# Optimization experiments

Hardware: AMD Instinct MI355X
Metric: run time of the kernel (lower is better)

## Reference

```python
import jax, jax.numpy as jnp
import numpy as np

B, L, NT = 4, 512, 20
H, DK, DM = 6, 10, 60  # heads, d_k, d_model (=embedding_dim+1)
ED = 59


def setup_inputs() -> dict:
    key = jax.random.key(0)
    ks = jax.random.split(key, 12)
    # event_seqs[..., 0] = event times (increasing), event_seqs[..., 1] = event type id stored as float
    times = jnp.cumsum(jax.random.uniform(ks[0], (B, L + 1)), axis=1)
    types = jax.random.randint(ks[1], (B, L + 1), 0, NT).astype(jnp.float32)
    event_seqs = jnp.stack([times, types], axis=-1)  # [B, L+1, 2]
    # causal (subsequent) mask, no padding -> lower-triangular [B, L, L]
    src_mask = jnp.broadcast_to(jnp.tril(jnp.ones((L, L), dtype=bool)), (B, L, L))
    w = lambda k, s: jax.random.normal(k, s, dtype=jnp.float32) * 0.1
    return dict(
        event_seqs=event_seqs, src_mask=src_mask,
        embed_w=w(ks[2], (ED, NT)),
        q_w=w(ks[3], (DM, DM)), q_b=jnp.zeros((DM,), jnp.float32),
        k_w=w(ks[4], (DM, DM)), k_b=jnp.zeros((DM,), jnp.float32),
        v_w=w(ks[5], (DM, DM)), v_b=jnp.zeros((DM,), jnp.float32),
        alpha_w=w(ks[6], (DK, DK * H // 2)), alpha_b=jnp.zeros((DK,), jnp.float32),
        gamma_w=w(ks[7], (DK, DK * H // 2)), gamma_b=jnp.zeros((DK,), jnp.float32),
        mu_w=w(ks[8], (DK, DM)), mu_b=jnp.zeros((DK,), jnp.float32),
    )


def reference(event_seqs, src_mask, embed_w, q_w, q_b, k_w, k_b, v_w, v_b,
              alpha_w, alpha_b, gamma_w, gamma_b, mu_w, mu_b):
    b = event_seqs.shape[0]
    # temporal feature: dt between consecutive events (ts padded with leading 0)
    ts = jnp.pad(event_seqs[:, :, 0], ((0, 0), (1, 0)))  # [B, T+1]
    dt = ts[:, 1:] - ts[:, :-1]                           # [B, T]
    temp_feat = dt[:, :-1, None]                          # [B, L, 1]
    types = event_seqs[:, :-1, 1].astype(jnp.int32)       # [B, L]
    type_feat = jax.nn.one_hot(types, NT, dtype=jnp.float32) @ embed_w.T  # [B, L, ED]
    feat = jnp.concatenate([temp_feat, type_feat], axis=-1)  # [B, L, DM]

    def heads(x, w, bias):
        return (x @ w.T + bias).reshape(b, L, H, DK).transpose(0, 2, 1, 3)  # [B,H,L,DK]

    q = heads(feat, q_w, q_b)
    k = heads(feat, k_w, k_b)
    v = heads(feat, v_w, v_b)

    mask4 = src_mask[:, None, :, :]  # [B,1,L,L]
    scores = jnp.einsum('bhid,bhjd->bhij', q, k) / np.sqrt(DK).astype(np.float32)
    scores = jnp.where(mask4, scores, -1e9)
    p_attn = jax.nn.softmax(scores, axis=-1)
    p_attn = jnp.where(mask4, p_attn, 0.0)               # [B,H,L,L]
    v_mu_pre = jnp.einsum('bhij,bhjd->bhid', p_attn, v)  # [B,H,L,DK]

    # per-pair attn * value, split heads in half (faithful to torch view semantics)
    prod = p_attn[..., None] * v[:, :, None, :, :]       # [B,H,L,L,DK]
    hh = H // 2
    x_alpha = prod[:, :hh].reshape(b, L, L, hh * DK)     # raw C-order reshape == torch .view
    x_gamma = prod[:, hh:].reshape(b, L, L, hh * DK)

    v_alpha = jax.nn.softplus(x_alpha @ alpha_w.T + alpha_b)          # Softplus(beta=1)
    v_gamma = jax.nn.softplus(10.0 * (x_gamma @ gamma_w.T + gamma_b)) / 10.0  # Softplus(beta=10)
    pair_mask = src_mask[..., None]                      # [B,L,L,1]
    v_alpha = jnp.where(pair_mask, v_alpha, 0.0)
    v_gamma = jnp.where(pair_mask, v_gamma, 0.0)

    v_mu = jax.nn.sigmoid(v_mu_pre.transpose(0, 2, 1, 3).reshape(b, L, DM) @ mu_w.T + mu_b)  # [B,L,DK]
    return (v_mu, v_alpha, v_gamma)
```

## Files before the change

kernel.cpp:

```cpp
#include <hip/hip_runtime.h>
#include <hip/hip_bf16.h>

#define BB 4
#define LL 512
#define NTYPES 20
#define HH 6
#define DKK 10
#define DMM 60
#define PROW 516
#define NWROW 516

__device__ __forceinline__ float softplus_fast(float x) {
    return fmaxf(x, 0.0f) + __logf(1.0f + __expf(-fabsf(x)));
}

__global__ void ishp_qkv(const float* __restrict__ ev,
                         const float* __restrict__ embed_w,
                         const float* __restrict__ qw, const float* __restrict__ qb,
                         const float* __restrict__ kw, const float* __restrict__ kb,
                         const float* __restrict__ vw, const float* __restrict__ vb,
                         const float* __restrict__ aw, const float* __restrict__ gw,
                         float* __restrict__ q, float* __restrict__ kT, float* __restrict__ vT,
                         float* __restrict__ Wbuf)
{
    int pos = blockIdx.x;
    int b = pos >> 9, l = pos & 511;
    __shared__ float feat[DMM];
    __shared__ float sv[DMM];
    int t = threadIdx.x;
    if (t == 0) {
        float t1 = ev[(b * (LL + 1) + l) * 2 + 0];
        float t0 = (l > 0) ? ev[(b * (LL + 1) + l - 1) * 2 + 0] : 0.0f;
        feat[0] = t1 - t0;
    } else if (t < DMM) {
        int type = (int)ev[(b * (LL + 1) + l) * 2 + 1];
        feat[t] = embed_w[(t - 1) * NTYPES + type];
    }
    __syncthreads();
    if (t < 3 * DMM) {
        int which = t / DMM;
        int m = t - which * DMM;
        const float* w  = which == 0 ? qw : which == 1 ? kw : vw;
        const float* bs = which == 0 ? qb : which == 1 ? kb : vb;
        float s = bs[m];
        #pragma unroll
        for (int c = 0; c < DMM; ++c) s += feat[c] * w[m * DMM + c];
        int h = m / DKK, d = m - h * DKK;
        if (which == 0)      q [((b * HH + h) * LL + l) * DKK + d] = s;
        else if (which == 1) kT[((b * HH + h) * DKK + d) * LL + l] = s;
        else {
            vT[((b * HH + h) * DKK + d) * LL + l] = s;
            sv[m] = s;
        }
    }
    __syncthreads();
    if (t < 180) {
        int kk = t % 10;
        int u = t / 10;
        int h  = u % 3;
        int cc = (u / 3) % 3;
        int mat = u / 9;
        const float* w = mat ? gw : aw;
        float s = 0.0f;
        #pragma unroll
        for (int d = 0; d < DKK; ++d) s += w[kk * 30 + cc * 10 + d] * sv[(h + 3 * mat) * DKK + d];
        int slot = (l % 3) * 172 + l / 3;
        Wbuf[((size_t)((((mat * 3 + cc) * 4 + b) * 3 + h) * 10 + kk)) * NWROW + slot] = s;
    }
}

__global__ __launch_bounds__(128) void ishp_attn(const float* __restrict__ q,
                                                 const float* __restrict__ kT,
                                                 const float* __restrict__ vT,
                                                 __hip_bfloat16* __restrict__ pbuf,
                                                 float* __restrict__ vmupre)
{
    int wid  = threadIdx.x >> 6;
    int lane = threadIdx.x & 63;
    int gw = blockIdx.x * 2 + wid;
    int bh = gw >> 8;
    int ib = gw & 255;
    int i0 = ib * 2, i1 = i0 + 1;
    const float* kT_ = kT + (size_t)bh * DKK * LL;
    const float* vT_ = vT + (size_t)bh * DKK * LL;

    float q0[DKK], q1[DKK];
    #pragma unroll
    for (int d = 0; d < DKK; ++d) {
        q0[d] = q[((size_t)bh * LL + i0) * DKK + d];
        q1[d] = q[((size_t)bh * LL + i1) * DKK + d];
    }

    const float scale = 0.31622776601683794f;
    int nchunk = (i1 >> 6) + 1;

    float e0[8], e1[8];
    float S0 = 0.0f, S1 = 0.0f;
    #pragma unroll
    for (int c = 0; c < 8; ++c) {
        e0[c] = 0.0f; e1[c] = 0.0f;
        if (c < nchunk) {
            int j = c * 64 + lane;
            float d0 = 0.0f, d1 = 0.0f;
            #pragma unroll
            for (int d = 0; d < DKK; ++d) {
                float kd = kT_[d * LL + j];
                d0 += q0[d] * kd;
                d1 += q1[d] * kd;
            }
            if (j <= i0) e0[c] = __expf(d0 * scale);
            if (j <= i1) e1[c] = __expf(d1 * scale);
            S0 += e0[c]; S1 += e1[c];
        }
    }
    #pragma unroll
    for (int off = 32; off >= 1; off >>= 1) {
        S0 += __shfl_xor(S0, off, 64);
        S1 += __shfl_xor(S1, off, 64);
    }
    float inv0 = 1.0f / S0, inv1 = 1.0f / S1;

    __hip_bfloat16* prow0 = pbuf + (size_t)(bh * LL + i0) * PROW;
    __hip_bfloat16* prow1 = pbuf + (size_t)(bh * LL + i1) * PROW;
    #pragma unroll
    for (int c = 0; c < 8; ++c) {
        if (c < nchunk) {
            int j = c * 64 + lane;
            int slot = (j % 3) * 172 + j / 3;
            if (j <= i0) prow0[slot] = __float2bfloat16(e0[c] * inv0);
            if (j <= i1) prow1[slot] = __float2bfloat16(e1[c] * inv1);
        }
    }

    float acc0[DKK], acc1[DKK];
    #pragma unroll
    for (int d = 0; d < DKK; ++d) { acc0[d] = 0.0f; acc1[d] = 0.0f; }
    #pragma unroll
    for (int c = 0; c < 8; ++c) {
        if (c < nchunk) {
            int j = c * 64 + lane;
            #pragma unroll
            for (int d = 0; d < DKK; ++d) {
                float vd = vT_[d * LL + j];
                acc0[d] += e0[c] * vd;
                acc1[d] += e1[c] * vd;
            }
        }
    }
    #pragma unroll
    for (int d = 0; d < DKK; ++d) {
        float a0 = acc0[d], a1 = acc1[d];
        #pragma unroll
        for (int off = 32; off >= 1; off >>= 1) {
            a0 += __shfl_xor(a0, off, 64);
            a1 += __shfl_xor(a1, off, 64);
        }
        acc0[d] = a0; acc1[d] = a1;
    }
    if (lane == 0) {
        #pragma unroll
        for (int d = 0; d < DKK; ++d) {
            vmupre[((size_t)bh * LL + i0) * DKK + d] = acc0[d] * inv0;
            vmupre[((size_t)bh * LL + i1) * DKK + d] = acc1[d] * inv1;
        }
    }
}

__global__ __launch_bounds__(256) void ishp_ag(const __hip_bfloat16* __restrict__ pbuf,
                                               const float* __restrict__ Wbuf,
                                               const float* __restrict__ ab,
                                               const float* __restrict__ gb,
                                               const float* __restrict__ vmupre,
                                               const float* __restrict__ muw,
                                               const float* __restrict__ mub,
                                               float* __restrict__ out_mu,
                                               float* __restrict__ outA,
                                               float* __restrict__ outG)
{
    __shared__ float sA[2560];
    __shared__ float sG[2560];
    int tid = threadIdx.x;
    int pos = blockIdx.x * 256 + tid;
    int b  = pos >> 18;
    int i2 = (pos >> 9) & 511;
    int j2 = pos & 511;

    float ra[DKK], rg[DKK];
    if (j2 > i2) {
        #pragma unroll
        for (int kk = 0; kk < DKK; ++kk) { ra[kk] = 0.0f; rg[kk] = 0.0f; }
    } else {
        #pragma unroll
        for (int kk = 0; kk < DKK; ++kk) { ra[kk] = ab[kk]; rg[kk] = gb[kk]; }
        #pragma unroll
        for (int cc = 0; cc < 3; ++cc) {
            int u = 3 * j2 + cc;
            int sel = u >> 9;
            int j = u & 511;
            int hi = 3 * i2 + sel;
            int h = hi >> 9;
            int i = hi & 511;
            int jq = j / 3;
            int r = j - 3 * jq;
            int slot = r * 172 + jq;
            float pa = 0.0f, pg = 0.0f;
            if (j <= i) {
                pa = __bfloat162float(pbuf[(size_t)((b * HH + h) * LL + i) * PROW + slot]);
                pg = __bfloat162float(pbuf[(size_t)((b * HH + h + 3) * LL + i) * PROW + slot]);
            }
            const float* Wa = Wbuf + ((size_t)(((0 + cc) * 4 + b) * 3 + h) * 10) * NWROW + slot;
            const float* Wg = Wbuf + ((size_t)(((3 + cc) * 4 + b) * 3 + h) * 10) * NWROW + slot;
            #pragma unroll
            for (int kk = 0; kk < DKK; ++kk) {
                ra[kk] += pa * Wa[kk * NWROW];
                rg[kk] += pg * Wg[kk * NWROW];
            }
        }
        #pragma unroll
        for (int kk = 0; kk < DKK; ++kk) {
            ra[kk] = softplus_fast(ra[kk]);
            rg[kk] = softplus_fast(10.0f * rg[kk]) * 0.1f;
        }
    }
    #pragma unroll
    for (int kk = 0; kk < DKK; ++kk) { sA[tid * 10 + kk] = ra[kk]; sG[tid * 10 + kk] = rg[kk]; }
    __syncthreads();

    size_t base = (size_t)blockIdx.x * 2560;
    #pragma unroll
    for (int it = 0; it < 3; ++it) {
        int idx = it * 1024 + tid * 4;
        if (idx < 2560) {
            *reinterpret_cast<float4*>(outA + base + idx) = *reinterpret_cast<const float4*>(&sA[idx]);
            *reinterpret_cast<float4*>(outG + base + idx) = *reinterpret_cast<const float4*>(&sG[idx]);
        }
    }

    if (blockIdx.x < 8) {
        int mpos = blockIdx.x * 256 + tid;
        int mb = mpos >> 9, ml = mpos & 511;
        float y[DKK];
        #pragma unroll
        for (int kk = 0; kk < DKK; ++kk) y[kk] = mub[kk];
        for (int c = 0; c < DMM; ++c) {
            int h = c / DKK, d = c - h * DKK;
            float xc = vmupre[((mb * HH + h) * LL + ml) * DKK + d];
            #pragma unroll
            for (int kk = 0; kk < DKK; ++kk) y[kk] += xc * muw[kk * DMM + c];
        }
        #pragma unroll
        for (int kk = 0; kk < DKK; ++kk)
            out_mu[(size_t)mpos * DKK + kk] = 1.0f / (1.0f + __expf(-y[kk]));
    }
}

extern "C" void kernel_launch(void* const* d_in, const int* in_sizes, int n_in,
                              void* d_out, int out_size, void* d_ws, size_t ws_size,
                              hipStream_t stream) {
    const void *ev = 0, *emb = 0, *muw = 0;
    const void *w3[3] = {0, 0, 0}, *b3[3] = {0, 0, 0};
    const void *w300[2] = {0, 0};
    const void *b10[3] = {0, 0, 0};
    int n3 = 0, nb3 = 0, n300 = 0, n10 = 0;
    for (int i = 0; i < n_in; ++i) {
        int s = in_sizes[i];
        if      (s == 4104) ev  = d_in[i];
        else if (s == 1180) emb = d_in[i];
        else if (s == 600)  muw = d_in[i];
        else if (s == 3600) { if (n3  < 3) w3[n3++]   = d_in[i]; }
        else if (s == 60)   { if (nb3 < 3) b3[nb3++]  = d_in[i]; }
        else if (s == 300)  { if (n300< 2) w300[n300++]=d_in[i]; }
        else if (s == 10)   { if (n10 < 3) b10[n10++] = d_in[i]; }
    }

    float* ws = (float*)d_ws;
    float* q = ws;
    float* kT = q + 122880;
    float* vT = kT + 122880;
    float* vmupre = vT + 122880;
    float* Wbuf = vmupre + 122880;
    __hip_bfloat16* pbuf = (__hip_bfloat16*)(Wbuf + 371520);

    float* out = (float*)d_out;
    float* out_mu = out;
    float* out_a  = out + 20480;
    float* out_g  = out + 20480 + 10485760;

    ishp_qkv<<<BB * LL, 192, 0, stream>>>((const float*)ev, (const float*)emb,
        (const float*)w3[0], (const float*)b3[0],
        (const float*)w3[1], (const float*)b3[1],
        (const float*)w3[2], (const float*)b3[2],
        (const float*)w300[0], (const float*)w300[1],
        q, kT, vT, Wbuf);
    ishp_attn<<<(BB * HH * LL) / 4, 128, 0, stream>>>(q, kT, vT, pbuf, vmupre);
    ishp_ag<<<(BB * LL * LL) / 256, 256, 0, stream>>>(pbuf, Wbuf,
        (const float*)b10[0], (const float*)b10[1], vmupre,
        (const float*)muw, (const float*)b10[2], out_mu, out_a, out_g);
}
```

Baseline: 60.52 us.

## Fuse attention softmax into alpha/gamma kernel and precompute type projection table

The attention kernel and the alpha/gamma projection kernel are merged into one kernel per (batch, output row). It recomputes the six needed attention rows into shared memory and consumes them directly, which removes the bf16 probability buffer round-trip through global memory. Separately, the QKV projection is replaced by a lookup in a small precomputed table of per-type projections plus a dt-scaled column, turning the 60-term dot products into one fused multiply-add. The exchange is that each block recomputes six attention rows of 512 dot products, so softmax work is duplicated across blocks. It also adds two extra small kernel launches.

```diff
diff --git a/kernel.cpp b/kernel.cpp
--- a/kernel.cpp
+++ b/kernel.cpp
@@ -7,44 +7,72 @@
 #define HH 6
 #define DKK 10
 #define DMM 60
-#define PROW 516
 #define NWROW 516
 
 __device__ __forceinline__ float softplus_fast(float x) {
     return fmaxf(x, 0.0f) + __logf(1.0f + __expf(-fabsf(x)));
 }
 
-__global__ void ishp_qkv(const float* __restrict__ ev,
-                         const float* __restrict__ embed_w,
+__device__ __forceinline__ void rowinfo(int b, int i2, int r, int& bh, int& i) {
+    int sel = (r < 3) ? r : r - 3;
+    int hi = 3 * i2 + sel;
+    int h = hi >> 9;
+    i = hi & 511;
+    bh = b * HH + h + ((r < 3) ? 0 : 3);
+}
+
+__global__ void ishp_tab(const float* __restrict__ emb,
                          const float* __restrict__ qw, const float* __restrict__ qb,
                          const float* __restrict__ kw, const float* __restrict__ kb,
                          const float* __restrict__ vw, const float* __restrict__ vb,
+                         float* __restrict__ Ptab)
+{
+    int idx = blockIdx.x * 256 + threadIdx.x;
+    if (idx < 3600) {
+        int which = idx / 1200;
+        int rem = idx - which * 1200;
+        int type = rem / 60;
+        int m = rem - type * 60;
+        const float* w  = which == 0 ? qw : which == 1 ? kw : vw;
+        const float* bs = which == 0 ? qb : which == 1 ? kb : vb;
+        float s = bs[m];
+        #pragma unroll
+        for (int c = 1; c < DMM; ++c) s += w[m * DMM + c] * emb[(c - 1) * NTYPES + type];
+        Ptab[idx] = s;
+    } else if (idx < 3780) {
+        int t = idx - 3600;
+        int which = t / 60;
+        int m = t - which * 60;
+        const float* w = which == 0 ? qw : which == 1 ? kw : vw;
+        Ptab[idx] = w[m * DMM];
+    }
+}
+
+__global__ void ishp_qkv(const float* __restrict__ ev,
+                         const float* __restrict__ Ptab,
                          const float* __restrict__ aw, const float* __restrict__ gw,
                          float* __restrict__ q, float* __restrict__ kT, float* __restrict__ vT,
                          float* __restrict__ Wbuf)
 {
     int pos = blockIdx.x;
     int b = pos >> 9, l = pos & 511;
-    __shared__ float feat[DMM];
     __shared__ float sv[DMM];
+    __shared__ float dtS;
+    __shared__ int typeS;
     int t = threadIdx.x;
     if (t == 0) {
         float t1 = ev[(b * (LL + 1) + l) * 2 + 0];
         float t0 = (l > 0) ? ev[(b * (LL + 1) + l - 1) * 2 + 0] : 0.0f;
-        feat[0] = t1 - t0;
-    } else if (t < DMM) {
-        int type = (int)ev[(b * (LL + 1) + l) * 2 + 1];
-        feat[t] = embed_w[(t - 1) * NTYPES + type];
-    }
-    __syncthreads();
-    if (t < 3 * DMM) {
+        dtS = t1 - t0;
+        typeS = (int)ev[(b * (LL + 1) + l) * 2 + 1];
+    }
+    __syncthreads();
+    float dt = dtS;
+    int type = typeS;
+    if (t < 180) {
         int which = t / DMM;
         int m = t - which * DMM;
-        const float* w  = which == 0 ? qw : which == 1 ? kw : vw;
-        const float* bs = which == 0 ? qb : which == 1 ? kb : vb;
-        float s = bs[m];
-        #pragma unroll
-        for (int c = 0; c < DMM; ++c) s += feat[c] * w[m * DMM + c];
+        float s = Ptab[which * 1200 + type * 60 + m] + dt * Ptab[3600 + which * 60 + m];
         int h = m / DKK, d = m - h * DKK;
         if (which == 0)      q [((b * HH + h) * LL + l) * DKK + d] = s;
         else if (which == 1) kT[((b * HH + h) * DKK + d) * LL + l] = s;
@@ -69,122 +97,83 @@
     }
 }
 
-__global__ __launch_bounds__(128) void ishp_attn(const float* __restrict__ q,
-                                                 const float* __restrict__ kT,
-                                                 const float* __restrict__ vT,
-                                                 __hip_bfloat16* __restrict__ pbuf,
-                                                 float* __restrict__ vmupre)
-{
-    int wid  = threadIdx.x >> 6;
-    int lane = threadIdx.x & 63;
-    int gw = blockIdx.x * 2 + wid;
-    int bh = gw >> 8;
-    int ib = gw & 255;
-    int i0 = ib * 2, i1 = i0 + 1;
-    const float* kT_ = kT + (size_t)bh * DKK * LL;
-    const float* vT_ = vT + (size_t)bh * DKK * LL;
-
-    float q0[DKK], q1[DKK];
-    #pragma unroll
-    for (int d = 0; d < DKK; ++d) {
-        q0[d] = q[((size_t)bh * LL + i0) * DKK + d];
-        q1[d] = q[((size_t)bh * LL + i1) * DKK + d];
-    }
-
+__global__ __launch_bounds__(512) void ishp_fused(const float* __restrict__ q,
+                                                  const float* __restrict__ kT,
+                                                  const float* __restrict__ vT,
+                                                  const float* __restrict__ Wbuf,
+                                                  const float* __restrict__ ab,
+                                                  const float* __restrict__ gb,
+                                                  float* __restrict__ vmupre,
+                                                  float* __restrict__ outA,
+                                                  float* __restrict__ outG)
+{
+    __shared__ float smem[10240];
+    __shared__ float sq[6][DKK];
+    __shared__ float invS[6];
+    __shared__ float wred[8][6];
+
+    int blk = blockIdx.x;
+    int b = blk >> 9, i2 = blk & 511;
+    int tid = threadIdx.x;
+    int lane = tid & 63;
+    int wv = tid >> 6;
     const float scale = 0.31622776601683794f;
-    int nchunk = (i1 >> 6) + 1;
-
-    float e0[8], e1[8];
-    float S0 = 0.0f, S1 = 0.0f;
-    #pragma unroll
-    for (int c = 0; c < 8; ++c) {
-        e0[c] = 0.0f; e1[c] = 0.0f;
-        if (c < nchunk) {
-            int j = c * 64 + lane;
-            float d0 = 0.0f, d1 = 0.0f;
-            #pragma unroll
-            for (int d = 0; d < DKK; ++d) {
-                float kd = kT_[d * LL + j];
-                d0 += q0[d] * kd;
-                d1 += q1[d] * kd;
-            }
-            if (j <= i0) e0[c] = __expf(d0 * scale);
-            if (j <= i1) e1[c] = __expf(d1 * scale);
-            S0 += e0[c]; S1 += e1[c];
-        }
-    }
-    #pragma unroll
-    for (int off = 32; off >= 1; off >>= 1) {
-        S0 += __shfl_xor(S0, off, 64);
-        S1 += __shfl_xor(S1, off, 64);
-    }
-    float inv0 = 1.0f / S0, inv1 = 1.0f / S1;
-
-    __hip_bfloat16* prow0 = pbuf + (size_t)(bh * LL + i0) * PROW;
-    __hip_bfloat16* prow1 = pbuf + (size_t)(bh * LL + i1) * PROW;
-    #pragma unroll
-    for (int c = 0; c < 8; ++c) {
-        if (c < nchunk) {
-            int j = c * 64 + lane;
-            int slot = (j % 3) * 172 + j / 3;
-            if (j <= i0) prow0[slot] = __float2bfloat16(e0[c] * inv0);
-            if (j <= i1) prow1[slot] = __float2bfloat16(e1[c] * inv1);
-        }
-    }
-
-    float acc0[DKK], acc1[DKK];
-    #pragma unroll
-    for (int d = 0; d < DKK; ++d) { acc0[d] = 0.0f; acc1[d] = 0.0f; }
-    #pragma unroll
-    for (int c = 0; c < 8; ++c) {
-        if (c < nchunk) {
-            int j = c * 64 + lane;
-            #pragma unroll
-            for (int d = 0; d < DKK; ++d) {
-                float vd = vT_[d * LL + j];
-                acc0[d] += e0[c] * vd;
-                acc1[d] += e1[c] * vd;
-            }
-        }
-    }
-    #pragma unroll
-    for (int d = 0; d < DKK; ++d) {
-        float a0 = acc0[d], a1 = acc1[d];
-        #pragma unroll
-        for (int off = 32; off >= 1; off >>= 1) {
-            a0 += __shfl_xor(a0, off, 64);
-            a1 += __shfl_xor(a1, off, 64);
-        }
-        acc0[d] = a0; acc1[d] = a1;
-    }
+
+    if (tid < 60) {
+        int r = tid / DKK, d = tid - (tid / DKK) * DKK;
+        int bh, i;
+        rowinfo(b, i2, r, bh, i);
+        sq[r][d] = q[((size_t)bh * LL + i) * DKK + d];
+    }
+    __syncthreads();
+
+    float ereg[6];
+    #pragma unroll
+    for (int r = 0; r < 6; ++r) {
+        int bh, i;
+        rowinfo(b, i2, r, bh, i);
+        const float* kb_ = kT + (size_t)bh * DKK * LL;
+        float dot = 0.0f;
+        #pragma unroll
+        for (int d = 0; d < DKK; ++d) dot += sq[r][d] * kb_[d * LL + tid];
+        float e = (tid <= i) ? __expf(dot * scale) : 0.0f;
+        smem[r * LL + tid] = e;
+        ereg[r] = e;
+    }
+    #pragma unroll
+    for (int r = 0; r < 6; ++r)
+        #pragma unroll
+        for (int off = 32; off >= 1; off >>= 1) ereg[r] += __shfl_xor(ereg[r], off, 64);
     if (lane == 0) {
         #pragma unroll
-        for (int d = 0; d < DKK; ++d) {
-            vmupre[((size_t)bh * LL + i0) * DKK + d] = acc0[d] * inv0;
-            vmupre[((size_t)bh * LL + i1) * DKK + d] = acc1[d] * inv1;
-        }
-    }
-}
-
-__global__ __launch_bounds__(256) void ishp_ag(const __hip_bfloat16* __restrict__ pbuf,
-                                               const float* __restrict__ Wbuf,
-                                               const float* __restrict__ ab,
-                                               const float* __restrict__ gb,
-                                               const float* __restrict__ vmupre,
-                                               const float* __restrict__ muw,
-                                               const float* __restrict__ mub,
-                                               float* __restrict__ out_mu,
-                                               float* __restrict__ outA,
-                                               float* __restrict__ outG)
-{
-    __shared__ float sA[2560];
-    __shared__ float sG[2560];
-    int tid = threadIdx.x;
-    int pos = blockIdx.x * 256 + tid;
-    int b  = pos >> 18;
-    int i2 = (pos >> 9) & 511;
-    int j2 = pos & 511;
-
+        for (int r = 0; r < 6; ++r) wred[wv][r] = ereg[r];
+    }
+    __syncthreads();
+    if (tid < 6) {
+        float s = 0.0f;
+        #pragma unroll
+        for (int w = 0; w < 8; ++w) s += wred[w][tid];
+        invS[tid] = 1.0f / s;
+    }
+    __syncthreads();
+
+    for (int task = wv; task < 60; task += 8) {
+        int r = task / DKK, d = task - (task / DKK) * DKK;
+        int bh, i;
+        rowinfo(b, i2, r, bh, i);
+        const float* vb_ = vT + ((size_t)bh * DKK + d) * LL;
+        float s = 0.0f;
+        #pragma unroll
+        for (int u = 0; u < 8; ++u) {
+            int j = lane + 64 * u;
+            s += smem[r * LL + j] * vb_[j];
+        }
+        #pragma unroll
+        for (int off = 32; off >= 1; off >>= 1) s += __shfl_xor(s, off, 64);
+        if (lane == 0) vmupre[((size_t)bh * LL + i) * DKK + d] = s * invS[r];
+    }
+
+    int j2 = tid;
     float ra[DKK], rg[DKK];
     if (j2 > i2) {
         #pragma unroll
@@ -199,15 +188,10 @@
             int j = u & 511;
             int hi = 3 * i2 + sel;
             int h = hi >> 9;
-            int i = hi & 511;
+            float pa = smem[sel * LL + j] * invS[sel];
+            float pg = smem[(3 + sel) * LL + j] * invS[3 + sel];
             int jq = j / 3;
-            int r = j - 3 * jq;
-            int slot = r * 172 + jq;
-            float pa = 0.0f, pg = 0.0f;
-            if (j <= i) {
-                pa = __bfloat162float(pbuf[(size_t)((b * HH + h) * LL + i) * PROW + slot]);
-                pg = __bfloat162float(pbuf[(size_t)((b * HH + h + 3) * LL + i) * PROW + slot]);
-            }
+            int slot = (j - 3 * jq) * 172 + jq;
             const float* Wa = Wbuf + ((size_t)(((0 + cc) * 4 + b) * 3 + h) * 10) * NWROW + slot;
             const float* Wg = Wbuf + ((size_t)(((3 + cc) * 4 + b) * 3 + h) * 10) * NWROW + slot;
             #pragma unroll
@@ -222,36 +206,44 @@
             rg[kk] = softplus_fast(10.0f * rg[kk]) * 0.1f;
         }
     }
-    #pragma unroll
-    for (int kk = 0; kk < DKK; ++kk) { sA[tid * 10 + kk] = ra[kk]; sG[tid * 10 + kk] = rg[kk]; }
-    __syncthreads();
-
-    size_t base = (size_t)blockIdx.x * 2560;
+    __syncthreads();
+    #pragma unroll
+    for (int kk = 0; kk < DKK; ++kk) {
+        smem[j2 * DKK + kk] = ra[kk];
+        smem[5120 + j2 * DKK + kk] = rg[kk];
+    }
+    __syncthreads();
+
+    size_t base = (size_t)blk * 5120;
     #pragma unroll
     for (int it = 0; it < 3; ++it) {
-        int idx = it * 1024 + tid * 4;
-        if (idx < 2560) {
-            *reinterpret_cast<float4*>(outA + base + idx) = *reinterpret_cast<const float4*>(&sA[idx]);
-            *reinterpret_cast<float4*>(outG + base + idx) = *reinterpret_cast<const float4*>(&sG[idx]);
-        }
-    }
-
-    if (blockIdx.x < 8) {
-        int mpos = blockIdx.x * 256 + tid;
-        int mb = mpos >> 9, ml = mpos & 511;
-        float y[DKK];
-        #pragma unroll
-        for (int kk = 0; kk < DKK; ++kk) y[kk] = mub[kk];
-        for (int c = 0; c < DMM; ++c) {
-            int h = c / DKK, d = c - h * DKK;
-            float xc = vmupre[((mb * HH + h) * LL + ml) * DKK + d];
-            #pragma unroll
-            for (int kk = 0; kk < DKK; ++kk) y[kk] += xc * muw[kk * DMM + c];
-        }
-        #pragma unroll
-        for (int kk = 0; kk < DKK; ++kk)
-            out_mu[(size_t)mpos * DKK + kk] = 1.0f / (1.0f + __expf(-y[kk]));
-    }
+        int idx = it * 2048 + tid * 4;
+        if (idx < 5120) {
+            *reinterpret_cast<float4*>(outA + base + idx) = *reinterpret_cast<const float4*>(&smem[idx]);
+            *reinterpret_cast<float4*>(outG + base + idx) = *reinterpret_cast<const float4*>(&smem[5120 + idx]);
+        }
+    }
+}
+
+__global__ void ishp_mu(const float* __restrict__ vmupre,
+                        const float* __restrict__ muw, const float* __restrict__ mub,
+                        float* __restrict__ out0)
+{
+    int pos = blockIdx.x * 256 + threadIdx.x;
+    if (pos >= BB * LL) return;
+    int b = pos >> 9, l = pos & 511;
+    float y[DKK];
+    #pragma unroll
+    for (int kk = 0; kk < DKK; ++kk) y[kk] = mub[kk];
+    for (int c = 0; c < DMM; ++c) {
+        int h = c / DKK, d = c - h * DKK;
+        float xc = vmupre[((b * HH + h) * LL + l) * DKK + d];
+        #pragma unroll
+        for (int kk = 0; kk < DKK; ++kk) y[kk] += xc * muw[kk * DMM + c];
+    }
+    #pragma unroll
+    for (int kk = 0; kk < DKK; ++kk)
+        out0[(size_t)pos * DKK + kk] = 1.0f / (1.0f + __expf(-y[kk]));
 }
 
 extern "C" void kernel_launch(void* const* d_in, const int* in_sizes, int n_in,
@@ -279,21 +271,20 @@
     float* vT = kT + 122880;
     float* vmupre = vT + 122880;
     float* Wbuf = vmupre + 122880;
-    __hip_bfloat16* pbuf = (__hip_bfloat16*)(Wbuf + 371520);
+    float* Ptab = Wbuf + 371520;
 
     float* out = (float*)d_out;
     float* out_mu = out;
     float* out_a  = out + 20480;
     float* out_g  = out + 20480 + 10485760;
 
-    ishp_qkv<<<BB * LL, 192, 0, stream>>>((const float*)ev, (const float*)emb,
+    ishp_tab<<<15, 256, 0, stream>>>((const float*)emb,
         (const float*)w3[0], (const float*)b3[0],
         (const float*)w3[1], (const float*)b3[1],
-        (const float*)w3[2], (const float*)b3[2],
-        (const float*)w300[0], (const float*)w300[1],
-        q, kT, vT, Wbuf);
-    ishp_attn<<<(BB * HH * LL) / 4, 128, 0, stream>>>(q, kT, vT, pbuf, vmupre);
-    ishp_ag<<<(BB * LL * LL) / 256, 256, 0, stream>>>(pbuf, Wbuf,
-        (const float*)b10[0], (const float*)b10[1], vmupre,
-        (const float*)muw, (const float*)b10[2], out_mu, out_a, out_g);
-}
+        (const float*)w3[2], (const float*)b3[2], Ptab);
+    ishp_qkv<<<BB * LL, 192, 0, stream>>>((const float*)ev, Ptab,
+        (const float*)w300[0], (const float*)w300[1], q, kT, vT, Wbuf);
+    ishp_fused<<<BB * LL, 512, 0, stream>>>(q, kT, vT, Wbuf,
+        (const float*)b10[0], (const float*)b10[1], vmupre, out_a, out_g);
+    ishp_mu<<<8, 256, 0, stream>>>(vmupre, (const float*)muw, (const float*)b10[2], out_mu);
+}
```

Measured after the change: 77.57 us. 1.28x slower.
